# Performance work log

Measured on AMD Instinct MI355X. Metric: run time of the kernel, lower is better.

## Reference

```python
import jax, jax.numpy as jnp
import numpy as np

B, N, D = 4, 2048, 1024
H, HD = 16, 64
S = 11  # n_scales
D4 = jnp.array([0.4829629131445341, 0.8365163037378079,
                0.2241438680420134, -0.1294095225512604], dtype=jnp.float32)


def _causal_dilated_d4(f, d):
    """Causal depthwise D4 conv with dilation d along axis 2. f: [B,H,N,HD].
    Matches torch F.pad(x,(3d,0)) + F.conv1d(dilation=d, groups=C):
    y[n] = sum_t D4[t] * f[n - (3-t)*d]."""
    n = f.shape[2]
    fp = jnp.pad(f, ((0, 0), (0, 0), (3 * d, 0), (0, 0)))
    return (D4[0] * fp[:, :, 0:n, :]
            + D4[1] * fp[:, :, d:d + n, :]
            + D4[2] * fp[:, :, 2 * d:2 * d + n, :]
            + D4[3] * fp[:, :, 3 * d:3 * d + n, :])


def setup_inputs() -> dict:
    key = jax.random.key(0)
    ks = jax.random.split(key, 10)
    s = 0.02
    return {
        "x": jax.random.normal(ks[0], (B, N, D), dtype=jnp.float32),
        "Wqkv": jax.random.normal(ks[1], (3 * D, D), dtype=jnp.float32) * s,
        "bqkv": jnp.zeros((3 * D,), dtype=jnp.float32),
        "Wo": jax.random.normal(ks[2], (D, D), dtype=jnp.float32) * s,
        "bo": jnp.zeros((D,), dtype=jnp.float32),
        "Wg": jax.random.normal(ks[3], (D, D), dtype=jnp.float32) * s,
        "bg": jnp.full((D,), 2.0, dtype=jnp.float32),
        "scale_gain": jnp.zeros((S, H), dtype=jnp.float32),
        "Wqs": jax.random.normal(ks[4], (S, HD), dtype=jnp.float32) * 0.01,
        "field_coupling": jnp.eye(H, dtype=jnp.float32)
        + 0.01 * jax.random.normal(ks[5], (H, H), dtype=jnp.float32),
    }


def reference(x, Wqkv, bqkv, Wo, bo, Wg, bg, scale_gain, Wqs, field_coupling):
    b, n, d = x.shape
    qkv = x @ Wqkv.T + bqkv                          # [B,N,3D]
    q, k, v = jnp.split(qkv, 3, axis=-1)
    q = q.reshape(b, n, H, HD).transpose(0, 2, 1, 3)  # [B,H,N,HD]
    k = k.reshape(b, n, H, HD).transpose(0, 2, 1, 3)
    v = v.reshape(b, n, H, HD).transpose(0, 2, 1, 3)

    # per-position scale gains: learned prior + query-conditioned offset
    q_offset = jnp.einsum('bhnd,sd->bhns', q, Wqs)    # [B,H,N,S]
    prior = scale_gain.T[None, :, None, :]            # [1,H,1,S]
    gains = jax.nn.softmax(q_offset + prior, axis=-1)

    # deposit: field[i] = V[i] * ||K[i]||
    k_mag = jnp.linalg.norm(k, axis=-1, keepdims=True)
    field = v * k_mag                                 # [B,H,N,HD]

    # propagate: causal multiscale dilated D4 conv, gain-weighted accumulate
    out_field = jnp.zeros_like(field)
    for j in range(S):
        y = _causal_dilated_d4(field, 1 << j)
        out_field = out_field + gains[:, :, :, j:j + 1] * y

    coupling = jax.nn.softmax(field_coupling, axis=-1)
    out_field = jnp.einsum('ij,bjnd->bind', coupling, out_field)

    gate = jax.nn.sigmoid(x @ Wg.T + bg)              # [B,N,D]
    gathered = out_field.transpose(0, 2, 1, 3).reshape(b, n, d)
    return (gathered * gate) @ Wo.T + bo
```

## Files before the change

kernel.cpp:

```cpp
#include <hip/hip_runtime.h>
#include <hip/hip_bf16.h>
#include <stdint.h>
#include <math.h>

#define BB 4
#define NN 2048
#define DD 1024
#define HH 16
#define HDD 64
#define SS 11

#define D4_0 0.4829629131445341f
#define D4_1 0.8365163037378079f
#define D4_2 0.2241438680420134f
#define D4_3 (-0.1294095225512604f)

typedef __bf16 bf16_t;
typedef __bf16 bf16x4_t __attribute__((ext_vector_type(4)));
typedef __bf16 bf16x8_t __attribute__((ext_vector_type(8)));
typedef float f32x4_t __attribute__((ext_vector_type(4)));

__global__ __launch_bounds__(256) void cvt_all_k(const float* __restrict__ s0,
                                                 const float* __restrict__ s1,
                                                 const float* __restrict__ s2,
                                                 const float* __restrict__ s3,
                                                 bf16_t* __restrict__ d0,
                                                 bf16_t* __restrict__ d1,
                                                 bf16_t* __restrict__ d2,
                                                 bf16_t* __restrict__ d3) {
  const int n0 = 2097152, n1 = 524288, n2 = 262144, n3 = 262144;
  int i = blockIdx.x * 256 + threadIdx.x;
  const float* s;
  bf16_t* d;
  if (i < n0) { s = s0; d = d0; }
  else if (i < n0 + n1) { i -= n0; s = s1; d = d1; }
  else if (i < n0 + n1 + n2) { i -= n0 + n1; s = s2; d = d2; }
  else { i -= n0 + n1 + n2; if (i >= n3) return; s = s3; d = d3; }
  f32x4_t v = ((const f32x4_t*)s)[i];
  bf16x4_t o;
  o[0] = (bf16_t)v[0]; o[1] = (bf16_t)v[1]; o[2] = (bf16_t)v[2]; o[3] = (bf16_t)v[3];
  ((bf16x4_t*)d)[i] = o;
}

__global__ __launch_bounds__(256) void wl_k(const float* __restrict__ Wqkv,
                                            const float* __restrict__ Wqs,
                                            const float* __restrict__ bqkv,
                                            bf16_t* __restrict__ Wlb,
                                            float* __restrict__ blv) {
  const int h = blockIdx.x;
  const int tid = threadIdx.x;
  const int d0 = tid * 4;
  float acc[SS][4];
#pragma unroll
  for (int s = 0; s < SS; s++)
#pragma unroll
    for (int j = 0; j < 4; j++) acc[s][j] = 0.f;
  for (int hd = 0; hd < 64; hd++) {
    f32x4_t w = *(const f32x4_t*)(Wqkv + (size_t)(h * 64 + hd) * 1024 + d0);
#pragma unroll
    for (int s = 0; s < SS; s++) {
      float qs = Wqs[s * 64 + hd];
#pragma unroll
      for (int j = 0; j < 4; j++) acc[s][j] += qs * w[j];
    }
  }
#pragma unroll
  for (int s = 0; s < SS; s++) {
    bf16x4_t o;
#pragma unroll
    for (int j = 0; j < 4; j++) o[j] = (bf16_t)acc[s][j];
    *(bf16x4_t*)(Wlb + (size_t)(h * SS + s) * 1024 + d0) = o;
  }
  if (tid < SS) {
    float b = 0.f;
    for (int hd = 0; hd < 64; hd++) b += Wqs[tid * 64 + hd] * bqkv[h * 64 + hd];
    blv[h * SS + tid] = b;
  }
  if (blockIdx.x == 0) {
    for (int i = tid; i < 80; i += 256) blv[176 + i] = 0.f;
    bf16x8_t z;
#pragma unroll
    for (int j = 0; j < 8; j++) z[j] = (bf16_t)0.f;
    bf16_t* pad = Wlb + 176ull * 1024;
    for (int i = tid; i < 80 * 1024 / 8; i += 256) ((bf16x8_t*)pad)[i] = z;
  }
}

__device__ __forceinline__ void gload16(const void* g, void* l) {
  __builtin_amdgcn_global_load_lds((__attribute__((address_space(1))) void*)(void*)g,
                                   (__attribute__((address_space(3))) void*)l,
                                   16, 0, 0);
}

__global__ __launch_bounds__(256) void gemm_a(const bf16_t* __restrict__ A,
                                              const bf16_t* __restrict__ Bw,
                                              const float* __restrict__ biasA,
                                              bf16_t* __restrict__ kb,
                                              bf16_t* __restrict__ vb,
                                              bf16_t* __restrict__ gateb,
                                              float* __restrict__ lgf) {
  __shared__ bf16_t As[128 * 64];
  __shared__ bf16_t Bs[128 * 64];
  const int K = 1024;

  const int tid = threadIdx.x;
  const int mtile = blockIdx.x / 26;
  const int ntile = blockIdx.x % 26;
  const int row0 = mtile << 7;
  const int col0 = ntile << 7;
  const int w = tid >> 6, lane = tid & 63;
  const int wm = w >> 1, wn = w & 1;
  const int m16 = lane & 15, quad = lane >> 4;

  f32x4_t acc[4][4];
#pragma unroll
  for (int i = 0; i < 4; i++)
#pragma unroll
    for (int jj = 0; jj < 4; jj++) acc[i][jj] = (f32x4_t){0.f, 0.f, 0.f, 0.f};

  for (int kb_ = 0; kb_ < K; kb_ += 64) {
    __syncthreads();
#pragma unroll
    for (int r = 0; r < 4; ++r) {
      int c = r * 256 + tid;
      int row = c >> 3, kc = c & 7;
      int swz = kc ^ (row & 7);
      const bf16_t* gpA = A + (size_t)(row0 + row) * K + kb_ + swz * 8;
      const bf16_t* gpB = Bw + (size_t)(col0 + row) * K + kb_ + swz * 8;
      bf16_t* lpA = As + (size_t)(r * 256 + (tid & 192)) * 8;
      bf16_t* lpB = Bs + (size_t)(r * 256 + (tid & 192)) * 8;
      gload16(gpA, lpA);
      gload16(gpB, lpB);
    }
    __syncthreads();

#pragma unroll
    for (int kk = 0; kk < 2; ++kk) {
      bf16x8_t af[4], bfr[4];
      const int kc = (kk << 2) + quad;
#pragma unroll
      for (int i = 0; i < 4; i++) {
        int arow = (wm << 6) + (i << 4) + m16;
        af[i] = *(const bf16x8_t*)(As + arow * 64 + ((kc ^ (arow & 7)) << 3));
        int brow = (wn << 6) + (i << 4) + m16;
        bfr[i] = *(const bf16x8_t*)(Bs + brow * 64 + ((kc ^ (brow & 7)) << 3));
      }
#pragma unroll
      for (int i = 0; i < 4; i++)
#pragma unroll
        for (int jj = 0; jj < 4; jj++)
          acc[i][jj] = __builtin_amdgcn_mfma_f32_16x16x32_bf16(af[i], bfr[jj], acc[i][jj], 0, 0, 0);
    }
  }

  const int region = ntile >> 3;
  if (region < 3) {
    bf16_t* outp = (region == 0) ? kb : (region == 1 ? vb : gateb);
    const int lc0 = col0 & 1023;
#pragma unroll
    for (int i = 0; i < 4; i++) {
#pragma unroll
      for (int jj = 0; jj < 4; jj++) {
        const int grow0 = row0 + (wm << 6) + (i << 4) + (quad << 2);
        const int coff = (wn << 6) + (jj << 4) + m16;
        const float bval = biasA[col0 + coff];
#pragma unroll
        for (int r = 0; r < 4; r++) {
          float val = acc[i][jj][r] + bval;
          if (region == 2) val = 1.f / (1.f + __expf(-val));
          outp[(size_t)(grow0 + r) * 1024 + lc0 + coff] = (bf16_t)val;
        }
      }
    }
  } else {
#pragma unroll
    for (int i = 0; i < 4; i++) {
#pragma unroll
      for (int jj = 0; jj < 4; jj++) {
        const int grow0 = row0 + (wm << 6) + (i << 4) + (quad << 2);
        const int gcol = col0 + (wn << 6) + (jj << 4) + m16;
        const float bval = biasA[gcol];
        const int c = gcol - 3072;
#pragma unroll
        for (int r = 0; r < 4; r++) {
          float val = acc[i][jj][r] + bval;
          if (c < 176) lgf[(size_t)(grow0 + r) * 176 + c] = val;
        }
      }
    }
  }
}

__global__ __launch_bounds__(256) void gemm_b(const bf16_t* __restrict__ A,
                                              const bf16_t* __restrict__ Bw,
                                              const float* __restrict__ bias,
                                              float* __restrict__ out,
                                              int M, int Nn, int K) {
  __shared__ bf16_t As[128 * 64];
  __shared__ bf16_t Bs[128 * 64];

  const int tid = threadIdx.x;
  const int ntiles = Nn >> 7;
  const int mtile = blockIdx.x / ntiles;
  const int ntile = blockIdx.x % ntiles;
  const int row0 = mtile << 7;
  const int col0 = ntile << 7;
  const int w = tid >> 6, lane = tid & 63;
  const int wm = w >> 1, wn = w & 1;
  const int m16 = lane & 15, quad = lane >> 4;

  f32x4_t acc[4][4];
#pragma unroll
  for (int i = 0; i < 4; i++)
#pragma unroll
    for (int jj = 0; jj < 4; jj++) acc[i][jj] = (f32x4_t){0.f, 0.f, 0.f, 0.f};

  for (int kb = 0; kb < K; kb += 64) {
    __syncthreads();
#pragma unroll
    for (int r = 0; r < 4; ++r) {
      int c = r * 256 + tid;
      int row = c >> 3, kc = c & 7;
      int swz = kc ^ (row & 7);
      const bf16_t* gpA = A + (size_t)(row0 + row) * K + kb + swz * 8;
      const bf16_t* gpB = Bw + (size_t)(col0 + row) * K + kb + swz * 8;
      bf16_t* lpA = As + (size_t)(r * 256 + (tid & 192)) * 8;
      bf16_t* lpB = Bs + (size_t)(r * 256 + (tid & 192)) * 8;
      gload16(gpA, lpA);
      gload16(gpB, lpB);
    }
    __syncthreads();

#pragma unroll
    for (int kk = 0; kk < 2; ++kk) {
      bf16x8_t af[4], bfr[4];
      const int kc = (kk << 2) + quad;
#pragma unroll
      for (int i = 0; i < 4; i++) {
        int arow = (wm << 6) + (i << 4) + m16;
        af[i] = *(const bf16x8_t*)(As + arow * 64 + ((kc ^ (arow & 7)) << 3));
        int brow = (wn << 6) + (i << 4) + m16;
        bfr[i] = *(const bf16x8_t*)(Bs + brow * 64 + ((kc ^ (brow & 7)) << 3));
      }
#pragma unroll
      for (int i = 0; i < 4; i++)
#pragma unroll
        for (int jj = 0; jj < 4; jj++)
          acc[i][jj] = __builtin_amdgcn_mfma_f32_16x16x32_bf16(af[i], bfr[jj], acc[i][jj], 0, 0, 0);
    }
  }

#pragma unroll
  for (int i = 0; i < 4; i++) {
#pragma unroll
    for (int jj = 0; jj < 4; jj++) {
      const int grow0 = row0 + (wm << 6) + (i << 4) + (quad << 2);
      const int gcol = col0 + (wn << 6) + (jj << 4) + m16;
      const float bval = bias[gcol];
#pragma unroll
      for (int r = 0; r < 4; r++)
        out[(size_t)(grow0 + r) * Nn + gcol] = acc[i][jj][r] + bval;
    }
  }
}

__global__ __launch_bounds__(256) void field_gains_k(const bf16_t* __restrict__ kb,
                                                     const bf16_t* __restrict__ vb,
                                                     const float* __restrict__ lgf,
                                                     const float* __restrict__ scale_gain,
                                                     bf16_t* __restrict__ fieldb,
                                                     float* __restrict__ gains) {
  __shared__ float skmag[4 * 16];
  const int tid = threadIdx.x;
  const int w = tid >> 6, lane = tid & 63;
  const int bn = blockIdx.x * 4 + w;
  const int b = bn >> 11, n_pos = bn & 2047;
  const int m16 = lane & 15, quad = lane >> 4;
  const bf16_t* kp = kb + (size_t)bn * 1024;

  bf16x8_t ak[2];
#pragma unroll
  for (int it = 0; it < 2; it++)
    ak[it] = *(const bf16x8_t*)(kp + m16 * 64 + it * 32 + quad * 8);

  f32x4_t acc_k = (f32x4_t){0.f, 0.f, 0.f, 0.f};
#pragma unroll
  for (int it = 0; it < 2; it++)
    acc_k = __builtin_amdgcn_mfma_f32_16x16x32_bf16(ak[it], ak[it], acc_k, 0, 0, 0);

#pragma unroll
  for (int r = 0; r < 4; r++) {
    if (m16 == quad * 4 + r) skmag[w * 16 + m16] = sqrtf(fmaxf(acc_k[r], 0.f));
  }
  __syncthreads();

#pragma unroll
  for (int h = 0; h < 16; h++) {
    const float km = skmag[w * 16 + h];
    const float v = (float)vb[(size_t)bn * 1024 + h * 64 + lane];
    fieldb[((size_t)(b * 16 + h) * 2048 + n_pos) * 64 + lane] = (bf16_t)(v * km);
  }

  if (lane < 16) {
    const int head = lane;
    float lg[SS];
    float mx = -1e30f;
#pragma unroll
    for (int s = 0; s < SS; s++) {
      lg[s] = lgf[(size_t)bn * 176 + head * SS + s] + scale_gain[s * 16 + head];
      mx = fmaxf(mx, lg[s]);
    }
    float se = 0.f;
#pragma unroll
    for (int s = 0; s < SS; s++) { lg[s] = __expf(lg[s] - mx); se += lg[s]; }
    const float inv = 1.f / se;
    float* gp = gains + ((size_t)(b * 16 + head) * 2048 + n_pos) * SS;
#pragma unroll
    for (int s = 0; s < SS; s++) gp[s] = lg[s] * inv;
  }
}

__global__ __launch_bounds__(256) void conv_k(const bf16_t* __restrict__ field,
                                              const float* __restrict__ gains,
                                              bf16_t* __restrict__ facc) {
  __shared__ float sg[32 * SS];
  const int tid = threadIdx.x;
  const int blk = blockIdx.x;
  const int bh = blk & 63;
  const int ntile = blk >> 6;
  const int n0 = ntile * 32;

  for (int i = tid; i < 32 * SS; i += 256)
    sg[i] = gains[((size_t)bh * 2048 + n0) * SS + i];
  __syncthreads();

  const int w = tid >> 6, lane = tid & 63;
  const int nsub = lane >> 3, c = lane & 7;
  const int ln = w * 8 + nsub;
  const int n = n0 + ln;
  const bf16_t* frow = field + (size_t)bh * 2048 * 64;

  float g[SS];
#pragma unroll
  for (int s = 0; s < SS; s++) g[s] = sg[ln * SS + s];

  float acc[8];
  {
    bf16x8_t f0 = *(const bf16x8_t*)(frow + (size_t)n * 64 + c * 8);
#pragma unroll
    for (int q = 0; q < 8; q++) acc[q] = D4_3 * (float)f0[q];
  }
#pragma unroll
  for (int j = 0; j < 11; j++) {
    float wgt = D4_2 * g[j];
    if (j >= 1) wgt += D4_1 * g[j - 1];
    int rr = n - (1 << j);
    float wv = rr >= 0 ? wgt : 0.f;
    rr = rr >= 0 ? rr : 0;
    bf16x8_t fv = *(const bf16x8_t*)(frow + (size_t)rr * 64 + c * 8);
#pragma unroll
    for (int q = 0; q < 8; q++) acc[q] += wv * (float)fv[q];
  }
#pragma unroll
  for (int j = 0; j < 10; j++) {
    int rr = n - (3 << j);
    float wv = rr >= 0 ? (D4_0 * g[j]) : 0.f;
    rr = rr >= 0 ? rr : 0;
    bf16x8_t fv = *(const bf16x8_t*)(frow + (size_t)rr * 64 + c * 8);
#pragma unroll
    for (int q = 0; q < 8; q++) acc[q] += wv * (float)fv[q];
  }
  bf16x8_t o;
#pragma unroll
  for (int q = 0; q < 8; q++) o[q] = (bf16_t)acc[q];
  *(bf16x8_t*)(facc + ((size_t)bh * 2048 + n) * 64 + c * 8) = o;
}

__global__ __launch_bounds__(1024) void couple_gate_k(const bf16_t* __restrict__ facc,
                                                      const float* __restrict__ fcoup,
                                                      const bf16_t* __restrict__ gate,
                                                      bf16_t* __restrict__ gmat) {
  __shared__ float sacc[1024];
  __shared__ float sc[256];
  __shared__ float scn[256];
  const int tid = threadIdx.x;
  const int bn = blockIdx.x;
  const int b = bn >> 11, n = bn & 2047;
  if (tid < 256) sc[tid] = fcoup[tid];
  const int i = tid >> 6, hd = tid & 63;
  sacc[tid] = (float)facc[(((size_t)(b * 16 + i)) * 2048 + n) * 64 + hd];
  __syncthreads();
  if (tid < 16) {
    float row[16];
    float mx = -1e30f;
#pragma unroll
    for (int j = 0; j < 16; j++) { row[j] = sc[tid * 16 + j]; mx = fmaxf(mx, row[j]); }
    float se = 0.f;
#pragma unroll
    for (int j = 0; j < 16; j++) { row[j] = __expf(row[j] - mx); se += row[j]; }
    float inv = 1.f / se;
#pragma unroll
    for (int j = 0; j < 16; j++) scn[tid * 16 + j] = row[j] * inv;
  }
  __syncthreads();
  float s = 0.f;
#pragma unroll
  for (int j = 0; j < 16; j++) s += scn[i * 16 + j] * sacc[j * 64 + hd];
  const float gt = (float)gate[(size_t)bn * 1024 + tid];
  gmat[(size_t)bn * 1024 + tid] = (bf16_t)(s * gt);
}

extern "C" void kernel_launch(void* const* d_in, const int* in_sizes, int n_in,
                              void* d_out, int out_size, void* d_ws, size_t ws_size,
                              hipStream_t stream) {
  (void)in_sizes; (void)n_in; (void)out_size; (void)ws_size;
  const float* x = (const float*)d_in[0];
  const float* Wqkv = (const float*)d_in[1];
  const float* bqkv = (const float*)d_in[2];
  const float* Wo = (const float*)d_in[3];
  const float* bo = (const float*)d_in[4];
  const float* Wg = (const float*)d_in[5];
  const float* bg = (const float*)d_in[6];
  const float* scale_gain = (const float*)d_in[7];
  const float* Wqs = (const float*)d_in[8];
  const float* fcoup = (const float*)d_in[9];

  char* ws = (char*)d_ws;
  size_t off = 0;
  auto alloc = [&](size_t bytes) {
    void* p = ws + off;
    off += (bytes + 255) & ~(size_t)255;
    return p;
  };
  bf16_t* xb = (bf16_t*)alloc(8192ull * 1024 * 2);
  bf16_t* Wab = (bf16_t*)alloc(3328ull * 1024 * 2);
  bf16_t* Wob = (bf16_t*)alloc(1024ull * 1024 * 2);
  float* biasA = (float*)alloc(3328ull * 4);
  bf16_t* kbuf = (bf16_t*)alloc(8192ull * 1024 * 2);
  bf16_t* vb = (bf16_t*)alloc(8192ull * 1024 * 2);
  bf16_t* gateb = (bf16_t*)alloc(8192ull * 1024 * 2);
  float* lgf = (float*)alloc(8192ull * 176 * 4);
  bf16_t* fieldb = (bf16_t*)alloc(8388608ull * 2);
  float* gains = (float*)alloc(8192ull * 16 * SS * 4);
  bf16_t* facc = (bf16_t*)alloc(8388608ull * 2);
  bf16_t* gmat = (bf16_t*)alloc(8192ull * 1024 * 2);

  hipMemcpyAsync(biasA, bqkv + 1024, 1024 * 4, hipMemcpyDeviceToDevice, stream);
  hipMemcpyAsync(biasA + 1024, bqkv + 2048, 1024 * 4, hipMemcpyDeviceToDevice, stream);
  hipMemcpyAsync(biasA + 2048, bg, 1024 * 4, hipMemcpyDeviceToDevice, stream);

  cvt_all_k<<<12288, 256, 0, stream>>>(x, Wqkv + 1048576, Wg, Wo,
                                       xb, Wab, Wab + 2048ull * 1024, Wob);

  wl_k<<<16, 256, 0, stream>>>(Wqkv, Wqs, bqkv, Wab + 3072ull * 1024, biasA + 3072);

  gemm_a<<<64 * 26, 256, 0, stream>>>(xb, Wab, biasA, kbuf, vb, gateb, lgf);

  field_gains_k<<<2048, 256, 0, stream>>>(kbuf, vb, lgf, scale_gain, fieldb, gains);

  conv_k<<<4096, 256, 0, stream>>>(fieldb, gains, facc);

  couple_gate_k<<<8192, 1024, 0, stream>>>(facc, fcoup, gateb, gmat);

  gemm_b<<<64 * 8, 256, 0, stream>>>(gmat, Wob, bo, (float*)d_out, 8192, 1024, 1024);
}
```

Measured before the change: 298.0 us.

## Merge prep kernels and write GEMM output into one unified bf16 buffer

Combines the fp32→bf16 conversion, the Wqs-folded weight computation, the bias assembly and the zero padding into one prep kernel. This replaces three memcpys and two launches. The first GEMM now writes a single row-major bf16 output of width 3328 (k, v, gate, gain logits) with a simple epilogue, and downstream kernels read from it with strided offsets. The gain logits are now stored in bf16 instead of fp32, which slightly lowers their precision. The padded 80 columns are also written out, which adds some write traffic.

```diff
diff --git a/kernel.cpp b/kernel.cpp
--- a/kernel.cpp
+++ b/kernel.cpp
@@ -9,6 +9,7 @@
 #define HH 16
 #define HDD 64
 #define SS 11
+#define LDC 3328
 
 #define D4_0 0.4829629131445341f
 #define D4_1 0.8365163037378079f
@@ -20,68 +21,73 @@
 typedef __bf16 bf16x8_t __attribute__((ext_vector_type(8)));
 typedef float f32x4_t __attribute__((ext_vector_type(4)));
 
-__global__ __launch_bounds__(256) void cvt_all_k(const float* __restrict__ s0,
-                                                 const float* __restrict__ s1,
-                                                 const float* __restrict__ s2,
-                                                 const float* __restrict__ s3,
-                                                 bf16_t* __restrict__ d0,
-                                                 bf16_t* __restrict__ d1,
-                                                 bf16_t* __restrict__ d2,
-                                                 bf16_t* __restrict__ d3) {
-  const int n0 = 2097152, n1 = 524288, n2 = 262144, n3 = 262144;
-  int i = blockIdx.x * 256 + threadIdx.x;
-  const float* s;
-  bf16_t* d;
-  if (i < n0) { s = s0; d = d0; }
-  else if (i < n0 + n1) { i -= n0; s = s1; d = d1; }
-  else if (i < n0 + n1 + n2) { i -= n0 + n1; s = s2; d = d2; }
-  else { i -= n0 + n1 + n2; if (i >= n3) return; s = s3; d = d3; }
-  f32x4_t v = ((const f32x4_t*)s)[i];
-  bf16x4_t o;
-  o[0] = (bf16_t)v[0]; o[1] = (bf16_t)v[1]; o[2] = (bf16_t)v[2]; o[3] = (bf16_t)v[3];
-  ((bf16x4_t*)d)[i] = o;
-}
-
-__global__ __launch_bounds__(256) void wl_k(const float* __restrict__ Wqkv,
-                                            const float* __restrict__ Wqs,
-                                            const float* __restrict__ bqkv,
-                                            bf16_t* __restrict__ Wlb,
-                                            float* __restrict__ blv) {
-  const int h = blockIdx.x;
-  const int tid = threadIdx.x;
-  const int d0 = tid * 4;
-  float acc[SS][4];
-#pragma unroll
-  for (int s = 0; s < SS; s++)
-#pragma unroll
-    for (int j = 0; j < 4; j++) acc[s][j] = 0.f;
-  for (int hd = 0; hd < 64; hd++) {
-    f32x4_t w = *(const f32x4_t*)(Wqkv + (size_t)(h * 64 + hd) * 1024 + d0);
+__global__ __launch_bounds__(256) void prep_k(const float* __restrict__ x,
+                                              const float* __restrict__ Wqkv,
+                                              const float* __restrict__ Wqs,
+                                              const float* __restrict__ bqkv,
+                                              const float* __restrict__ Wg,
+                                              const float* __restrict__ Wo,
+                                              const float* __restrict__ bg,
+                                              bf16_t* __restrict__ xb,
+                                              bf16_t* __restrict__ Wab,
+                                              bf16_t* __restrict__ Wob,
+                                              float* __restrict__ biasA) {
+  const int blk = blockIdx.x;
+  const int tid = threadIdx.x;
+  if (blk < 12288) {
+    int i = blk * 256 + tid;
+    const int n0 = 2097152, n1 = 524288, n2 = 262144;
+    const float* s;
+    bf16_t* d;
+    if (i < n0) { s = x; d = xb; }
+    else if (i < n0 + n1) { i -= n0; s = Wqkv + 1048576; d = Wab; }
+    else if (i < n0 + n1 + n2) { i -= n0 + n1; s = Wg; d = Wab + 2048ull * 1024; }
+    else { i -= n0 + n1 + n2; s = Wo; d = Wob; }
+    f32x4_t v = ((const f32x4_t*)s)[i];
+    bf16x4_t o;
+    o[0] = (bf16_t)v[0]; o[1] = (bf16_t)v[1]; o[2] = (bf16_t)v[2]; o[3] = (bf16_t)v[3];
+    ((bf16x4_t*)d)[i] = o;
+  } else if (blk < 12304) {
+    const int h = blk - 12288;
+    const int d0 = tid * 4;
+    float acc[SS][4];
+#pragma unroll
+    for (int s = 0; s < SS; s++)
+#pragma unroll
+      for (int j = 0; j < 4; j++) acc[s][j] = 0.f;
+    for (int hd = 0; hd < 64; hd++) {
+      f32x4_t w = *(const f32x4_t*)(Wqkv + (size_t)(h * 64 + hd) * 1024 + d0);
+#pragma unroll
+      for (int s = 0; s < SS; s++) {
+        float qs = Wqs[s * 64 + hd];
+#pragma unroll
+        for (int j = 0; j < 4; j++) acc[s][j] += qs * w[j];
+      }
+    }
+    bf16_t* Wlb = Wab + 3072ull * 1024;
 #pragma unroll
     for (int s = 0; s < SS; s++) {
-      float qs = Wqs[s * 64 + hd];
-#pragma unroll
-      for (int j = 0; j < 4; j++) acc[s][j] += qs * w[j];
-    }
-  }
-#pragma unroll
-  for (int s = 0; s < SS; s++) {
-    bf16x4_t o;
-#pragma unroll
-    for (int j = 0; j < 4; j++) o[j] = (bf16_t)acc[s][j];
-    *(bf16x4_t*)(Wlb + (size_t)(h * SS + s) * 1024 + d0) = o;
-  }
-  if (tid < SS) {
-    float b = 0.f;
-    for (int hd = 0; hd < 64; hd++) b += Wqs[tid * 64 + hd] * bqkv[h * 64 + hd];
-    blv[h * SS + tid] = b;
-  }
-  if (blockIdx.x == 0) {
-    for (int i = tid; i < 80; i += 256) blv[176 + i] = 0.f;
+      bf16x4_t o;
+#pragma unroll
+      for (int j = 0; j < 4; j++) o[j] = (bf16_t)acc[s][j];
+      *(bf16x4_t*)(Wlb + (size_t)(h * SS + s) * 1024 + d0) = o;
+    }
+    if (tid < SS) {
+      float b = 0.f;
+      for (int hd = 0; hd < 64; hd++) b += Wqs[tid * 64 + hd] * bqkv[h * 64 + hd];
+      biasA[3072 + h * SS + tid] = b;
+    }
+  } else {
+    for (int i = tid; i < 1024; i += 256) {
+      biasA[i] = bqkv[1024 + i];
+      biasA[1024 + i] = bqkv[2048 + i];
+      biasA[2048 + i] = bg[i];
+    }
+    for (int i = tid; i < 80; i += 256) biasA[3072 + 176 + i] = 0.f;
     bf16x8_t z;
 #pragma unroll
     for (int j = 0; j < 8; j++) z[j] = (bf16_t)0.f;
-    bf16_t* pad = Wlb + 176ull * 1024;
+    bf16_t* pad = Wab + (3072ull + 176) * 1024;
     for (int i = tid; i < 80 * 1024 / 8; i += 256) ((bf16x8_t*)pad)[i] = z;
   }
 }
@@ -95,10 +101,7 @@
 __global__ __launch_bounds__(256) void gemm_a(const bf16_t* __restrict__ A,
                                               const bf16_t* __restrict__ Bw,
                                               const float* __restrict__ biasA,
-                                              bf16_t* __restrict__ kb,
-                                              bf16_t* __restrict__ vb,
-                                              bf16_t* __restrict__ gateb,
-                                              float* __restrict__ lgf) {
+                                              bf16_t* __restrict__ C) {
   __shared__ bf16_t As[128 * 64];
   __shared__ bf16_t Bs[128 * 64];
   const int K = 1024;
@@ -106,103 +109,6 @@
   const int tid = threadIdx.x;
   const int mtile = blockIdx.x / 26;
   const int ntile = blockIdx.x % 26;
-  const int row0 = mtile << 7;
-  const int col0 = ntile << 7;
-  const int w = tid >> 6, lane = tid & 63;
-  const int wm = w >> 1, wn = w & 1;
-  const int m16 = lane & 15, quad = lane >> 4;
-
-  f32x4_t acc[4][4];
-#pragma unroll
-  for (int i = 0; i < 4; i++)
-#pragma unroll
-    for (int jj = 0; jj < 4; jj++) acc[i][jj] = (f32x4_t){0.f, 0.f, 0.f, 0.f};
-
-  for (int kb_ = 0; kb_ < K; kb_ += 64) {
-    __syncthreads();
-#pragma unroll
-    for (int r = 0; r < 4; ++r) {
-      int c = r * 256 + tid;
-      int row = c >> 3, kc = c & 7;
-      int swz = kc ^ (row & 7);
-      const bf16_t* gpA = A + (size_t)(row0 + row) * K + kb_ + swz * 8;
-      const bf16_t* gpB = Bw + (size_t)(col0 + row) * K + kb_ + swz * 8;
-      bf16_t* lpA = As + (size_t)(r * 256 + (tid & 192)) * 8;
-      bf16_t* lpB = Bs + (size_t)(r * 256 + (tid & 192)) * 8;
-      gload16(gpA, lpA);
-      gload16(gpB, lpB);
-    }
-    __syncthreads();
-
-#pragma unroll
-    for (int kk = 0; kk < 2; ++kk) {
-      bf16x8_t af[4], bfr[4];
-      const int kc = (kk << 2) + quad;
-#pragma unroll
-      for (int i = 0; i < 4; i++) {
-        int arow = (wm << 6) + (i << 4) + m16;
-        af[i] = *(const bf16x8_t*)(As + arow * 64 + ((kc ^ (arow & 7)) << 3));
-        int brow = (wn << 6) + (i << 4) + m16;
-        bfr[i] = *(const bf16x8_t*)(Bs + brow * 64 + ((kc ^ (brow & 7)) << 3));
-      }
-#pragma unroll
-      for (int i = 0; i < 4; i++)
-#pragma unroll
-        for (int jj = 0; jj < 4; jj++)
-          acc[i][jj] = __builtin_amdgcn_mfma_f32_16x16x32_bf16(af[i], bfr[jj], acc[i][jj], 0, 0, 0);
-    }
-  }
-
-  const int region = ntile >> 3;
-  if (region < 3) {
-    bf16_t* outp = (region == 0) ? kb : (region == 1 ? vb : gateb);
-    const int lc0 = col0 & 1023;
-#pragma unroll
-    for (int i = 0; i < 4; i++) {
-#pragma unroll
-      for (int jj = 0; jj < 4; jj++) {
-        const int grow0 = row0 + (wm << 6) + (i << 4) + (quad << 2);
-        const int coff = (wn << 6) + (jj << 4) + m16;
-        const float bval = biasA[col0 + coff];
-#pragma unroll
-        for (int r = 0; r < 4; r++) {
-          float val = acc[i][jj][r] + bval;
-          if (region == 2) val = 1.f / (1.f + __expf(-val));
-          outp[(size_t)(grow0 + r) * 1024 + lc0 + coff] = (bf16_t)val;
-        }
-      }
-    }
-  } else {
-#pragma unroll
-    for (int i = 0; i < 4; i++) {
-#pragma unroll
-      for (int jj = 0; jj < 4; jj++) {
-        const int grow0 = row0 + (wm << 6) + (i << 4) + (quad << 2);
-        const int gcol = col0 + (wn << 6) + (jj << 4) + m16;
-        const float bval = biasA[gcol];
-        const int c = gcol - 3072;
-#pragma unroll
-        for (int r = 0; r < 4; r++) {
-          float val = acc[i][jj][r] + bval;
-          if (c < 176) lgf[(size_t)(grow0 + r) * 176 + c] = val;
-        }
-      }
-    }
-  }
-}
-
-__global__ __launch_bounds__(256) void gemm_b(const bf16_t* __restrict__ A,
-                                              const bf16_t* __restrict__ Bw,
-                                              const float* __restrict__ bias,
-                                              float* __restrict__ out,
-                                              int M, int Nn, int K) {
-  __shared__ bf16_t As[128 * 64];
-  __shared__ bf16_t Bs[128 * 64];
-
-  const int tid = threadIdx.x;
-  const int ntiles = Nn >> 7;
-  const int mtile = blockIdx.x / ntiles;
-  const int ntile = blockIdx.x % ntiles;
   const int row0 = mtile << 7;
   const int col0 = ntile << 7;
   const int w = tid >> 6, lane = tid & 63;
@@ -256,6 +162,83 @@
     for (int jj = 0; jj < 4; jj++) {
       const int grow0 = row0 + (wm << 6) + (i << 4) + (quad << 2);
       const int gcol = col0 + (wn << 6) + (jj << 4) + m16;
+      const float bval = biasA[gcol];
+      const bool isgate = (gcol >= 2048) && (gcol < 3072);
+#pragma unroll
+      for (int r = 0; r < 4; r++) {
+        float val = acc[i][jj][r] + bval;
+        if (isgate) val = 1.f / (1.f + __expf(-val));
+        C[(size_t)(grow0 + r) * LDC + gcol] = (bf16_t)val;
+      }
+    }
+  }
+}
+
+__global__ __launch_bounds__(256) void gemm_b(const bf16_t* __restrict__ A,
+                                              const bf16_t* __restrict__ Bw,
+                                              const float* __restrict__ bias,
+                                              float* __restrict__ out,
+                                              int M, int Nn, int K) {
+  __shared__ bf16_t As[128 * 64];
+  __shared__ bf16_t Bs[128 * 64];
+
+  const int tid = threadIdx.x;
+  const int ntiles = Nn >> 7;
+  const int mtile = blockIdx.x / ntiles;
+  const int ntile = blockIdx.x % ntiles;
+  const int row0 = mtile << 7;
+  const int col0 = ntile << 7;
+  const int w = tid >> 6, lane = tid & 63;
+  const int wm = w >> 1, wn = w & 1;
+  const int m16 = lane & 15, quad = lane >> 4;
+
+  f32x4_t acc[4][4];
+#pragma unroll
+  for (int i = 0; i < 4; i++)
+#pragma unroll
+    for (int jj = 0; jj < 4; jj++) acc[i][jj] = (f32x4_t){0.f, 0.f, 0.f, 0.f};
+
+  for (int kb = 0; kb < K; kb += 64) {
+    __syncthreads();
+#pragma unroll
+    for (int r = 0; r < 4; ++r) {
+      int c = r * 256 + tid;
+      int row = c >> 3, kc = c & 7;
+      int swz = kc ^ (row & 7);
+      const bf16_t* gpA = A + (size_t)(row0 + row) * K + kb + swz * 8;
+      const bf16_t* gpB = Bw + (size_t)(col0 + row) * K + kb + swz * 8;
+      bf16_t* lpA = As + (size_t)(r * 256 + (tid & 192)) * 8;
+      bf16_t* lpB = Bs + (size_t)(r * 256 + (tid & 192)) * 8;
+      gload16(gpA, lpA);
+      gload16(gpB, lpB);
+    }
+    __syncthreads();
+
+#pragma unroll
+    for (int kk = 0; kk < 2; ++kk) {
+      bf16x8_t af[4], bfr[4];
+      const int kc = (kk << 2) + quad;
+#pragma unroll
+      for (int i = 0; i < 4; i++) {
+        int arow = (wm << 6) + (i << 4) + m16;
+        af[i] = *(const bf16x8_t*)(As + arow * 64 + ((kc ^ (arow & 7)) << 3));
+        int brow = (wn << 6) + (i << 4) + m16;
+        bfr[i] = *(const bf16x8_t*)(Bs + brow * 64 + ((kc ^ (brow & 7)) << 3));
+      }
+#pragma unroll
+      for (int i = 0; i < 4; i++)
+#pragma unroll
+        for (int jj = 0; jj < 4; jj++)
+          acc[i][jj] = __builtin_amdgcn_mfma_f32_16x16x32_bf16(af[i], bfr[jj], acc[i][jj], 0, 0, 0);
+    }
+  }
+
+#pragma unroll
+  for (int i = 0; i < 4; i++) {
+#pragma unroll
+    for (int jj = 0; jj < 4; jj++) {
+      const int grow0 = row0 + (wm << 6) + (i << 4) + (quad << 2);
+      const int gcol = col0 + (wn << 6) + (jj << 4) + m16;
       const float bval = bias[gcol];
 #pragma unroll
       for (int r = 0; r < 4; r++)
@@ -264,9 +247,7 @@
   }
 }
 
-__global__ __launch_bounds__(256) void field_gains_k(const bf16_t* __restrict__ kb,
-                                                     const bf16_t* __restrict__ vb,
-                                                     const float* __restrict__ lgf,
+__global__ __launch_bounds__(256) void field_gains_k(const bf16_t* __restrict__ C,
                                                      const float* __restrict__ scale_gain,
                                                      bf16_t* __restrict__ fieldb,
                                                      float* __restrict__ gains) {
@@ -276,12 +257,12 @@
   const int bn = blockIdx.x * 4 + w;
   const int b = bn >> 11, n_pos = bn & 2047;
   const int m16 = lane & 15, quad = lane >> 4;
-  const bf16_t* kp = kb + (size_t)bn * 1024;
+  const bf16_t* cp = C + (size_t)bn * LDC;
 
   bf16x8_t ak[2];
 #pragma unroll
   for (int it = 0; it < 2; it++)
-    ak[it] = *(const bf16x8_t*)(kp + m16 * 64 + it * 32 + quad * 8);
+    ak[it] = *(const bf16x8_t*)(cp + m16 * 64 + it * 32 + quad * 8);
 
   f32x4_t acc_k = (f32x4_t){0.f, 0.f, 0.f, 0.f};
 #pragma unroll
@@ -297,17 +278,18 @@
 #pragma unroll
   for (int h = 0; h < 16; h++) {
     const float km = skmag[w * 16 + h];
-    const float v = (float)vb[(size_t)bn * 1024 + h * 64 + lane];
+    const float v = (float)cp[1024 + h * 64 + lane];
     fieldb[((size_t)(b * 16 + h) * 2048 + n_pos) * 64 + lane] = (bf16_t)(v * km);
   }
 
   if (lane < 16) {
     const int head = lane;
+    const bf16_t* lp = cp + 3072 + head * SS;
     float lg[SS];
     float mx = -1e30f;
 #pragma unroll
     for (int s = 0; s < SS; s++) {
-      lg[s] = lgf[(size_t)bn * 176 + head * SS + s] + scale_gain[s * 16 + head];
+      lg[s] = (float)lp[s] + scale_gain[s * 16 + head];
       mx = fmaxf(mx, lg[s]);
     }
     float se = 0.f;
@@ -378,7 +360,7 @@
 
 __global__ __launch_bounds__(1024) void couple_gate_k(const bf16_t* __restrict__ facc,
                                                       const float* __restrict__ fcoup,
-                                                      const bf16_t* __restrict__ gate,
+                                                      const bf16_t* __restrict__ C,
                                                       bf16_t* __restrict__ gmat) {
   __shared__ float sacc[1024];
   __shared__ float sc[256];
@@ -406,7 +388,7 @@
   float s = 0.f;
 #pragma unroll
   for (int j = 0; j < 16; j++) s += scn[i * 16 + j] * sacc[j * 64 + hd];
-  const float gt = (float)gate[(size_t)bn * 1024 + tid];
+  const float gt = (float)C[(size_t)bn * LDC + 2048 + tid];
   gmat[(size_t)bn * 1024 + tid] = (bf16_t)(s * gt);
 }
 
@@ -436,31 +418,21 @@
   bf16_t* Wab = (bf16_t*)alloc(3328ull * 1024 * 2);
   bf16_t* Wob = (bf16_t*)alloc(1024ull * 1024 * 2);
   float* biasA = (float*)alloc(3328ull * 4);
-  bf16_t* kbuf = (bf16_t*)alloc(8192ull * 1024 * 2);
-  bf16_t* vb = (bf16_t*)alloc(8192ull * 1024 * 2);
-  bf16_t* gateb = (bf16_t*)alloc(8192ull * 1024 * 2);
-  float* lgf = (float*)alloc(8192ull * 176 * 4);
+  bf16_t* C = (bf16_t*)alloc(8192ull * LDC * 2);
   bf16_t* fieldb = (bf16_t*)alloc(8388608ull * 2);
   float* gains = (float*)alloc(8192ull * 16 * SS * 4);
   bf16_t* facc = (bf16_t*)alloc(8388608ull * 2);
   bf16_t* gmat = (bf16_t*)alloc(8192ull * 1024 * 2);
 
-  hipMemcpyAsync(biasA, bqkv + 1024, 1024 * 4, hipMemcpyDeviceToDevice, stream);
-  hipMemcpyAsync(biasA + 1024, bqkv + 2048, 1024 * 4, hipMemcpyDeviceToDevice, stream);
-  hipMemcpyAsync(biasA + 2048, bg, 1024 * 4, hipMemcpyDeviceToDevice, stream);
-
-  cvt_all_k<<<12288, 256, 0, stream>>>(x, Wqkv + 1048576, Wg, Wo,
-                                       xb, Wab, Wab + 2048ull * 1024, Wob);
-
-  wl_k<<<16, 256, 0, stream>>>(Wqkv, Wqs, bqkv, Wab + 3072ull * 1024, biasA + 3072);
-
-  gemm_a<<<64 * 26, 256, 0, stream>>>(xb, Wab, biasA, kbuf, vb, gateb, lgf);
-
-  field_gains_k<<<2048, 256, 0, stream>>>(kbuf, vb, lgf, scale_gain, fieldb, gains);
+  prep_k<<<12305, 256, 0, stream>>>(x, Wqkv, Wqs, bqkv, Wg, Wo, bg, xb, Wab, Wob, biasA);
+
+  gemm_a<<<64 * 26, 256, 0, stream>>>(xb, Wab, biasA, C);
+
+  field_gains_k<<<2048, 256, 0, stream>>>(C, scale_gain, fieldb, gains);
 
   conv_k<<<4096, 256, 0, stream>>>(fieldb, gains, facc);
 
-  couple_gate_k<<<8192, 1024, 0, stream>>>(facc, fcoup, gateb, gmat);
+  couple_gate_k<<<8192, 1024, 0, stream>>>(facc, fcoup, C, gmat);
 
   gemm_b<<<64 * 8, 256, 0, stream>>>(gmat, Wob, bo, (float*)d_out, 8192, 1024, 1024);
 }
```

Result: no change. 295.0 us (-1.0%).
